# Kernel tuning notes

Hardware: AMD Instinct MI355X
Metric: run time of the kernel (lower is better)

The kernel has to match this reference:

```python
import jax, jax.numpy as jnp
import numpy as np

N_NODES = 100000
N_EDGES = 300000
N_GRAPHS = 2048
F_ATOM = 40
D_IN = 128    # GINInputSize
D_HID = 256   # GINHiddenSize
D_OUT = 512   # FPSize
D_TASK = 1    # OutputSize


def _glorot(key, shape):
    fan_in, fan_out = shape[0], shape[1]
    lim = (6.0 / (fan_in + fan_out)) ** 0.5
    return jax.random.uniform(key, shape, jnp.float32, -lim, lim)


def setup_inputs() -> dict:
    key = jax.random.key(0)
    ks = jax.random.split(key, 16)
    inp = {
        'x': jax.random.normal(ks[0], (N_NODES, F_ATOM), jnp.float32),
        'edge_index': jax.random.randint(ks[1], (2, N_EDGES), 0, N_NODES, jnp.int64),
        'batch': jnp.sort(jax.random.randint(ks[2], (N_NODES,), 0, N_GRAPHS, jnp.int64)),
        # NodeFeatEmbed: MLP([F_ATOM, D_IN]) == single Linear (plain_last)
        'W_embed': _glorot(ks[3], (F_ATOM, D_IN)),
        'b_embed': jnp.zeros((D_IN,), jnp.float32),
        # GINConv eps per layer (train_eps=False -> 0.0 constants)
        'eps': jnp.zeros((3,), jnp.float32),
        # layer 0: MLP([D_IN, D_HID, D_HID])
        'W1_0': _glorot(ks[4], (D_IN, D_HID)),  'b1_0': jnp.zeros((D_HID,), jnp.float32),
        'W2_0': _glorot(ks[5], (D_HID, D_HID)), 'b2_0': jnp.zeros((D_HID,), jnp.float32),
        # layer 1: MLP([D_HID, D_HID, D_HID])
        'W1_1': _glorot(ks[6], (D_HID, D_HID)), 'b1_1': jnp.zeros((D_HID,), jnp.float32),
        'W2_1': _glorot(ks[7], (D_HID, D_HID)), 'b2_1': jnp.zeros((D_HID,), jnp.float32),
        # layer 2 (last, maps to out_channels=FPSize): MLP([D_HID, D_OUT, D_OUT])
        'W1_2': _glorot(ks[8], (D_HID, D_OUT)), 'b1_2': jnp.zeros((D_OUT,), jnp.float32),
        'W2_2': _glorot(ks[9], (D_OUT, D_OUT)), 'b2_2': jnp.zeros((D_OUT,), jnp.float32),
        # task head
        'W_task': _glorot(ks[10], (D_OUT, D_TASK)),
        'b_task': jnp.zeros((D_TASK,), jnp.float32),
    }
    return inp


def _gin_forward(x, edge_index, batch, W_embed, b_embed, eps, layers, W_task, b_task):
    src, dst = edge_index[0], edge_index[1]
    # NodeFeatEmbed
    h = x @ W_embed + b_embed                                    # [N, D_IN]
    n_layers = len(layers)
    for l, (W1, b1, W2, b2) in enumerate(layers):
        # GINConv: MLP((1+eps)*h + sum_{j->i} h_j)
        agg = jax.ops.segment_sum(h[src], dst, num_segments=N_NODES)
        z = (1.0 + eps[l]) * h + agg
        h = jax.nn.relu(z @ W1 + b1) @ W2 + b2
        if l < n_layers - 1:                                     # inter-layer act (not after last)
            h = jax.nn.relu(h)
    # global_add_pool readout
    pooled = jax.ops.segment_sum(h, batch, num_segments=N_GRAPHS)  # [G, D_OUT]
    return pooled @ W_task + b_task                               # [G, D_TASK]


def reference(x, edge_index, batch, W_embed, b_embed, eps,
              W1_0, b1_0, W2_0, b2_0,
              W1_1, b1_1, W2_1, b2_1,
              W1_2, b1_2, W2_2, b2_2,
              W_task, b_task):
    layers = [(W1_0, b1_0, W2_0, b2_0), (W1_1, b1_1, W2_1, b2_1), (W1_2, b1_2, W2_2, b2_2)]
    return _gin_forward(x, edge_index, batch, W_embed, b_embed, eps, layers, W_task, b_task)
```

## Files before the change

kernel.cpp:

```cpp
#include <hip/hip_runtime.h>

#define N_NODES 100000
#define E_EDGES 300000
#define N_GRAPHS 2048

typedef float  floatx4 __attribute__((ext_vector_type(4)));
typedef short  shortx8 __attribute__((ext_vector_type(8)));

__device__ __forceinline__ float bf2f(unsigned short u) {
  return __uint_as_float(((unsigned int)u) << 16);
}
__device__ __forceinline__ unsigned short f2bf(float f) {
  unsigned int u = __float_as_uint(f);
  u += 0x7FFFu + ((u >> 16) & 1u);
  return (unsigned short)(u >> 16);
}

__device__ __forceinline__ void cp16(const void* g, void* l) {
  __builtin_amdgcn_global_load_lds(
      (const __attribute__((address_space(1))) unsigned int*)g,
      (__attribute__((address_space(3))) unsigned int*)l, 16, 0, 0);
}

struct PrepArgs {
  const float* W[4];
  unsigned short* Wt[4];
  int K[4];
  int N[4];
  const float* We;
  const float* be;
  const float* W1_0;
  unsigned short* WfT;
  const float* W2_2;
  const float* b2_2;
  const float* wtask;
  float* w2v;
  float* c2;
  float* nodedot;
  float* out;
  const float* b_task;
};

__global__ __launch_bounds__(256)
void prep_kernel(PrepArgs a) {
  const int blk = blockIdx.x;
  if (blk < 320) {
    int z, b;
    if (blk < 64)       { z = 0; b = blk; }
    else if (blk < 128) { z = 1; b = blk - 64; }
    else if (blk < 192) { z = 2; b = blk - 128; }
    else                { z = 3; b = blk - 192; }
    const int K = a.K[z], N = a.N[z];
    const int nt = N / 32;
    const int kb = (b / nt) * 32, nb = (b % nt) * 32;
    __shared__ unsigned short tile[32][33];
    const float* W = a.W[z];
    unsigned short* Wt = a.Wt[z];
    const int tx = threadIdx.x & 31, ty = threadIdx.x >> 5;
    for (int r = ty; r < 32; r += 8)
      tile[r][tx] = f2bf(W[(size_t)(kb + r) * N + nb + tx]);
    __syncthreads();
    for (int r = ty; r < 32; r += 8)
      Wt[(size_t)(nb + r) * K + kb + tx] = tile[tx][r];
  } else if (blk < 361) {
    const int k = blk - 320;
    const int n = threadIdx.x;
    if (k < 40) {
      float s = 0.f;
      for (int j = 0; j < 128; j++) s = fmaf(a.We[k * 128 + j], a.W1_0[(size_t)j * 256 + n], s);
      a.WfT[n * 64 + k] = f2bf(s);
    } else {
      float s = 0.f;
      for (int j = 0; j < 128; j++) s = fmaf(a.be[j], a.W1_0[(size_t)j * 256 + n], s);
      a.WfT[n * 64 + 40] = f2bf(s);
      for (int kk = 41; kk < 64; kk++) a.WfT[n * 64 + kk] = 0;
    }
  } else if (blk < 490) {
    const int p = blk - 361;
    const int lane = threadIdx.x & 63;
    const int wave = threadIdx.x >> 6;
    if (p < 128) {
      const int k = p * 4 + wave;
      const float* row = a.W2_2 + (size_t)k * 512 + lane * 8;
      float4 a0 = *(const float4*)(row);
      float4 a1 = *(const float4*)(row + 4);
      float4 w0 = *(const float4*)(a.wtask + lane * 8);
      float4 w1 = *(const float4*)(a.wtask + lane * 8 + 4);
      float s = a0.x * w0.x + a0.y * w0.y + a0.z * w0.z + a0.w * w0.w +
                a1.x * w1.x + a1.y * w1.y + a1.z * w1.z + a1.w * w1.w;
#pragma unroll
      for (int off = 32; off > 0; off >>= 1) s += __shfl_down(s, off);
      if (lane == 0) a.w2v[k] = s;
    } else if (wave == 0) {
      float4 a0 = *(const float4*)(a.b2_2 + lane * 8);
      float4 a1 = *(const float4*)(a.b2_2 + lane * 8 + 4);
      float4 w0 = *(const float4*)(a.wtask + lane * 8);
      float4 w1 = *(const float4*)(a.wtask + lane * 8 + 4);
      float s = a0.x * w0.x + a0.y * w0.y + a0.z * w0.z + a0.w * w0.w +
                a1.x * w1.x + a1.y * w1.y + a1.z * w1.z + a1.w * w1.w;
#pragma unroll
      for (int off = 32; off > 0; off >>= 1) s += __shfl_down(s, off);
      if (lane == 0) *a.c2 = s;
    }
  } else if (blk < 881) {
    int i = (blk - 490) * 256 + threadIdx.x;
    if (i < N_NODES) a.nodedot[i] = 0.f;
  } else {
    int g = (blk - 881) * 256 + threadIdx.x;
    if (g < N_GRAPHS) a.out[g] = a.b_task[0];
  }
}

__global__ __launch_bounds__(256)
void hist_kernel(const int* __restrict__ ei, int* __restrict__ deg) {
  int e = blockIdx.x * 256 + threadIdx.x;
  if (e < E_EDGES) atomicAdd(&deg[ei[E_EDGES + e]], 1);
}

__global__ __launch_bounds__(256)
void scan_blk_kernel(const int* __restrict__ in, int* __restrict__ out,
                     int* __restrict__ blk_sums, int n_in, int n_out) {
  __shared__ int sm[256];
  const int t = threadIdx.x;
  const int base = blockIdx.x * 1024 + t * 4;
  int d0 = (base + 0 < n_in) ? in[base + 0] : 0;
  int d1 = (base + 1 < n_in) ? in[base + 1] : 0;
  int d2 = (base + 2 < n_in) ? in[base + 2] : 0;
  int d3 = (base + 3 < n_in) ? in[base + 3] : 0;
  int s = d0 + d1 + d2 + d3;
  sm[t] = s;
  __syncthreads();
  for (int off = 1; off < 256; off <<= 1) {
    int v = (t >= off) ? sm[t - off] : 0;
    __syncthreads();
    sm[t] += v;
    __syncthreads();
  }
  int excl = sm[t] - s;
  if (base + 0 < n_out) out[base + 0] = excl;
  if (base + 1 < n_out) out[base + 1] = excl + d0;
  if (base + 2 < n_out) out[base + 2] = excl + d0 + d1;
  if (base + 3 < n_out) out[base + 3] = excl + d0 + d1 + d2;
  if (t == 255 && blk_sums) blk_sums[blockIdx.x] = sm[255];
}

__global__ __launch_bounds__(256)
void scan_fix_kernel(int* __restrict__ row_ptr, const int* __restrict__ blk_off,
                     int* __restrict__ cursor) {
  int i = blockIdx.x * 256 + threadIdx.x;
  if (i <= N_NODES) {
    int v = row_ptr[i] + blk_off[i >> 10];
    row_ptr[i] = v;
    if (i < N_NODES) cursor[i] = v;
  }
}

__global__ __launch_bounds__(256)
void fill_kernel(const int* __restrict__ ei, int* __restrict__ cursor,
                 int* __restrict__ csr_src) {
  int e = blockIdx.x * 256 + threadIdx.x;
  if (e < E_EDGES) {
    int d = ei[E_EDGES + e];
    int slot = atomicAdd(&cursor[d], 1);
    csr_src[slot] = ei[e];
  }
}

__global__ __launch_bounds__(256)
void gatherx_kernel(const float* __restrict__ X, unsigned short* __restrict__ G,
                    const int* __restrict__ row_ptr, const int* __restrict__ csr,
                    const float* __restrict__ eps) {
  const int node = blockIdx.x * 4 + (threadIdx.x >> 6);
  const int lane = threadIdx.x & 63;
  const float sc = 1.0f + eps[0];
  const int e0 = row_ptr[node];
  const int e1 = row_ptr[node + 1];
  float acc = 0.f;
  if (lane < 40) {
    acc = sc * X[(size_t)node * 40 + lane];
    int e = e0;
    for (; e + 4 <= e1; e += 4) {
      int s0 = csr[e], s1 = csr[e + 1], s2 = csr[e + 2], s3 = csr[e + 3];
      float a0 = X[(size_t)s0 * 40 + lane];
      float a1 = X[(size_t)s1 * 40 + lane];
      float a2 = X[(size_t)s2 * 40 + lane];
      float a3 = X[(size_t)s3 * 40 + lane];
      acc += (a0 + a1) + (a2 + a3);
    }
    for (; e < e1; e++)
      acc += X[(size_t)csr[e] * 40 + lane];
  } else if (lane == 40) {
    acc = sc + (float)(e1 - e0);
  }
  G[(size_t)node * 64 + lane] = f2bf(acc);
}

__global__ __launch_bounds__(256)
void gather_kernel(const unsigned short* __restrict__ H, unsigned short* __restrict__ Z,
                   const int* __restrict__ row_ptr, const int* __restrict__ csr,
                   const float* __restrict__ eps, int l) {
  const int node = blockIdx.x * 4 + (threadIdx.x >> 6);
  const int lane = threadIdx.x & 63;
  const int half = lane >> 5;
  const int hl = lane & 31;
  const float sc = 1.0f + eps[l];
  float acc[8];
#pragma unroll
  for (int k = 0; k < 8; k++) acc[k] = 0.f;

  if (half == 0) {
    uint4 v = *(const uint4*)(H + (size_t)node * 256 + hl * 8);
    acc[0] = sc * bf2f((unsigned short)(v.x & 0xFFFF));
    acc[1] = sc * bf2f((unsigned short)(v.x >> 16));
    acc[2] = sc * bf2f((unsigned short)(v.y & 0xFFFF));
    acc[3] = sc * bf2f((unsigned short)(v.y >> 16));
    acc[4] = sc * bf2f((unsigned short)(v.z & 0xFFFF));
    acc[5] = sc * bf2f((unsigned short)(v.z >> 16));
    acc[6] = sc * bf2f((unsigned short)(v.w & 0xFFFF));
    acc[7] = sc * bf2f((unsigned short)(v.w >> 16));
  }

  const int e0 = row_ptr[node];
  const int e1 = row_ptr[node + 1];
  int e = e0;
  for (; e + 2 <= e1; e += 2) {
    int s = csr[e + half];
    uint4 v = *(const uint4*)(H + (size_t)s * 256 + hl * 8);
    acc[0] += bf2f((unsigned short)(v.x & 0xFFFF));
    acc[1] += bf2f((unsigned short)(v.x >> 16));
    acc[2] += bf2f((unsigned short)(v.y & 0xFFFF));
    acc[3] += bf2f((unsigned short)(v.y >> 16));
    acc[4] += bf2f((unsigned short)(v.z & 0xFFFF));
    acc[5] += bf2f((unsigned short)(v.z >> 16));
    acc[6] += bf2f((unsigned short)(v.w & 0xFFFF));
    acc[7] += bf2f((unsigned short)(v.w >> 16));
  }
  if (e < e1 && half == 0) {
    int s = csr[e];
    uint4 v = *(const uint4*)(H + (size_t)s * 256 + hl * 8);
    acc[0] += bf2f((unsigned short)(v.x & 0xFFFF));
    acc[1] += bf2f((unsigned short)(v.x >> 16));
    acc[2] += bf2f((unsigned short)(v.y & 0xFFFF));
    acc[3] += bf2f((unsigned short)(v.y >> 16));
    acc[4] += bf2f((unsigned short)(v.z & 0xFFFF));
    acc[5] += bf2f((unsigned short)(v.z >> 16));
    acc[6] += bf2f((unsigned short)(v.w & 0xFFFF));
    acc[7] += bf2f((unsigned short)(v.w >> 16));
  }

#pragma unroll
  for (int k = 0; k < 8; k++) acc[k] += __shfl_down(acc[k], 32);

  if (half == 0) {
    unsigned short z[8];
#pragma unroll
    for (int k = 0; k < 8; k++) z[k] = f2bf(acc[k]);
    *(uint4*)(Z + (size_t)node * 256 + hl * 8) = *(const uint4*)z;
  }
}

template <int K1>
__global__ __launch_bounds__(256, 2)
void fused_mlp_kernel(const unsigned short* __restrict__ A,
                      const unsigned short* __restrict__ W1t,
                      const float* __restrict__ b1,
                      const unsigned short* __restrict__ W2t,
                      const float* __restrict__ b2,
                      unsigned short* __restrict__ H,
                      int M) {
  constexpr int ACH = K1 / 8;
  constexpr int ZP = (64 * ACH) / 256;
  constexpr int NT1 = K1 / 32;

  __shared__ unsigned short Bs[2][256 * 32];
  __shared__ unsigned short Ts[64 * 256];

  const int m0 = blockIdx.x * 64;
  const int tid = threadIdx.x;
  const int lane = tid & 63;
  const int wave = tid >> 6;
  const int fr = lane & 15;
  const int fq = lane >> 4;
  const int wn = wave * 64;

#pragma unroll
  for (int p = 0; p < ZP; p++) {
    int slot = p * 256 + tid;
    int row = slot / ACH;
    int cs = slot % ACH;
    int cg = cs ^ (row & 7);
    int grow = m0 + row;
    if (grow >= M) grow = M - 1;
    cp16(A + (size_t)grow * K1 + cg * 8, Ts + (size_t)(p * 256 + wn) * 8);
  }

  const int bn_ = tid >> 2;
  const int bc_ = tid & 3;
  const unsigned short* srcW1[4];
  const unsigned short* srcW2[4];
#pragma unroll
  for (int p = 0; p < 4; p++) {
    int n = p * 64 + bn_;
    int sw = (bc_ ^ ((n >> 1) & 3)) << 3;
    srcW1[p] = W1t + (size_t)n * K1 + sw;
    srcW2[p] = W2t + (size_t)n * 256 + sw;
  }

  int offB[4];
#pragma unroll
  for (int j = 0; j < 4; j++) {
    int n = wn + j * 16 + fr;
    offB[j] = n * 32 + ((fq ^ ((n >> 1) & 3)) << 3);
  }

#pragma unroll
  for (int p = 0; p < 4; p++)
    cp16(srcW1[p], &Bs[0][(size_t)(p * 256 + wn) * 8]);

  floatx4 acc[4][4];
#pragma unroll
  for (int i = 0; i < 4; i++)
#pragma unroll
    for (int j = 0; j < 4; j++) acc[i][j] = (floatx4){0.f, 0.f, 0.f, 0.f};

  __syncthreads();
  int buf = 0;

  for (int t = 0; t < NT1; t++) {
    if (t + 1 < NT1) {
#pragma unroll
      for (int p = 0; p < 4; p++)
        cp16(srcW1[p] + (t + 1) * 32, &Bs[buf ^ 1][(size_t)(p * 256 + wn) * 8]);
    } else {
#pragma unroll
      for (int p = 0; p < 4; p++)
        cp16(srcW2[p], &Bs[buf ^ 1][(size_t)(p * 256 + wn) * 8]);
    }
    shortx8 af[4], bv[4];
    const int kc = t * 4;
#pragma unroll
    for (int i = 0; i < 4; i++) {
      int row = i * 16 + fr;
      af[i] = *(const shortx8*)&Ts[row * K1 + (((kc + fq) ^ (fr & 7)) << 3)];
    }
#pragma unroll
    for (int j = 0; j < 4; j++) bv[j] = *(const shortx8*)&Bs[buf][offB[j]];
#pragma unroll
    for (int i = 0; i < 4; i++)
#pragma unroll
      for (int j = 0; j < 4; j++)
        acc[i][j] = __builtin_amdgcn_mfma_f32_16x16x32_bf16(af[i], bv[j], acc[i][j], 0, 0, 0);
    __syncthreads();
    buf ^= 1;
  }

#pragma unroll
  for (int j = 0; j < 4; j++) {
    int col = wn + j * 16 + fr;
    float bb = b1[col];
    int cgc = col >> 3, c7 = col & 7;
#pragma unroll
    for (int i = 0; i < 4; i++)
#pragma unroll
      for (int r = 0; r < 4; r++) {
        int row = i * 16 + fq * 4 + r;
        float v = fmaxf(acc[i][j][r] + bb, 0.f);
        Ts[row * 256 + (((cgc ^ (row & 7)) << 3) | c7)] = f2bf(v);
        acc[i][j][r] = 0.f;
      }
  }
  __syncthreads();

  for (int t = 0; t < 8; t++) {
    if (t + 1 < 8) {
#pragma unroll
      for (int p = 0; p < 4; p++)
        cp16(srcW2[p] + (t + 1) * 32, &Bs[buf ^ 1][(size_t)(p * 256 + wn) * 8]);
    }
    shortx8 af[4], bv[4];
    const int kc = t * 4;
#pragma unroll
    for (int i = 0; i < 4; i++) {
      int row = i * 16 + fr;
      af[i] = *(const shortx8*)&Ts[row * 256 + (((kc + fq) ^ (fr & 7)) << 3)];
    }
#pragma unroll
    for (int j = 0; j < 4; j++) bv[j] = *(const shortx8*)&Bs[buf][offB[j]];
#pragma unroll
    for (int i = 0; i < 4; i++)
#pragma unroll
      for (int j = 0; j < 4; j++)
        acc[i][j] = __builtin_amdgcn_mfma_f32_16x16x32_bf16(af[i], bv[j], acc[i][j], 0, 0, 0);
    __syncthreads();
    buf ^= 1;
  }

#pragma unroll
  for (int j = 0; j < 4; j++) {
    int col = wn + j * 16 + fr;
    float bb = b2[col];
    int cgc = col >> 3, c7 = col & 7;
#pragma unroll
    for (int i = 0; i < 4; i++)
#pragma unroll
      for (int r = 0; r < 4; r++) {
        int row = i * 16 + fq * 4 + r;
        float v = fmaxf(acc[i][j][r] + bb, 0.f);
        Ts[row * 256 + (((cgc ^ (row & 7)) << 3) | c7)] = f2bf(v);
      }
  }
  __syncthreads();
  const int r2 = tid >> 5;
  const int cg2 = tid & 31;
#pragma unroll
  for (int p = 0; p < 8; p++) {
    int row = p * 8 + r2;
    int grow = m0 + row;
    if (grow < M) {
      uint4 v = *(const uint4*)&Ts[row * 256 + ((cg2 ^ (row & 7)) << 3)];
      *(uint4*)&H[(size_t)grow * 256 + cg2 * 8] = v;
    }
  }
}

__global__ __launch_bounds__(256, 2)
void fused_dot_kernel(const unsigned short* __restrict__ A,
                      const unsigned short* __restrict__ W1t,
                      const float* __restrict__ b1,
                      const float* __restrict__ w2v,
                      float* __restrict__ nodedot4, int M) {
  __shared__ unsigned short Bs[2][256 * 32];
  __shared__ unsigned short Ts[64 * 256];

  const int m0 = blockIdx.x * 64;
  const int tid = threadIdx.x;
  const int lane = tid & 63;
  const int wave = tid >> 6;
  const int fr = lane & 15;
  const int fq = lane >> 4;
  const int wn = wave * 64;

#pragma unroll
  for (int p = 0; p < 8; p++) {
    int slot = p * 256 + tid;
    int row = slot >> 5;
    int cs = slot & 31;
    int cg = cs ^ (row & 7);
    int grow = m0 + row;
    if (grow >= M) grow = M - 1;
    cp16(A + (size_t)grow * 256 + cg * 8, Ts + (size_t)(p * 256 + wn) * 8);
  }

  const int bn_ = tid >> 2;
  const int bc_ = tid & 3;
  const unsigned short* srcW[4];
#pragma unroll
  for (int p = 0; p < 4; p++) {
    int n = p * 64 + bn_;
    srcW[p] = W1t + (size_t)n * 256 + ((bc_ ^ ((n >> 1) & 3)) << 3);
  }
  int offB[4];
#pragma unroll
  for (int j = 0; j < 4; j++) {
    int n = wn + j * 16 + fr;
    offB[j] = n * 32 + ((fq ^ ((n >> 1) & 3)) << 3);
  }

#pragma unroll
  for (int p = 0; p < 4; p++)
    cp16(srcW[p], &Bs[0][(size_t)(p * 256 + wn) * 8]);

  float pd[4][4];
#pragma unroll
  for (int i = 0; i < 4; i++)
#pragma unroll
    for (int r = 0; r < 4; r++) pd[i][r] = 0.f;

  floatx4 acc[4][4];
#pragma unroll
  for (int i = 0; i < 4; i++)
#pragma unroll
    for (int j = 0; j < 4; j++) acc[i][j] = (floatx4){0.f, 0.f, 0.f, 0.f};

  __syncthreads();
  int buf = 0;

  for (int s = 0; s < 16; s++) {
    int ns = s + 1;
    if (ns < 16) {
      const size_t off = (size_t)(ns >> 3) * 65536 + (size_t)(ns & 7) * 32;
#pragma unroll
      for (int p = 0; p < 4; p++)
        cp16(srcW[p] + off, &Bs[buf ^ 1][(size_t)(p * 256 + wn) * 8]);
    }
    shortx8 af[4], bv[4];
    const int kc = (s & 7) * 4;
#pragma unroll
    for (int i = 0; i < 4; i++) {
      int row = i * 16 + fr;
      af[i] = *(const shortx8*)&Ts[row * 256 + (((kc + fq) ^ (fr & 7)) << 3)];
    }
#pragma unroll
    for (int j = 0; j < 4; j++) bv[j] = *(const shortx8*)&Bs[buf][offB[j]];
#pragma unroll
    for (int i = 0; i < 4; i++)
#pragma unroll
      for (int j = 0; j < 4; j++)
        acc[i][j] = __builtin_amdgcn_mfma_f32_16x16x32_bf16(af[i], bv[j], acc[i][j], 0, 0, 0);
    __syncthreads();
    buf ^= 1;

    if ((s & 7) == 7) {
      const int nh = s >> 3;
#pragma unroll
      for (int j = 0; j < 4; j++) {
        int col = nh * 256 + wn + j * 16 + fr;
        float bb = b1[col];
        float wv = w2v[col];
#pragma unroll
        for (int i = 0; i < 4; i++)
#pragma unroll
          for (int r = 0; r < 4; r++) {
            pd[i][r] += fmaxf(acc[i][j][r] + bb, 0.f) * wv;
            acc[i][j][r] = 0.f;
          }
      }
    }
  }

#pragma unroll
  for (int i = 0; i < 4; i++)
#pragma unroll
    for (int r = 0; r < 4; r++) {
      float s = pd[i][r];
#pragma unroll
      for (int off = 1; off < 16; off <<= 1) s += __shfl_xor(s, off);
      if (fr == 0) {
        int row = m0 + i * 16 + fq * 4 + r;
        if (row < M) nodedot4[(size_t)wave * N_NODES + row] = s;
      }
    }
}

__global__ __launch_bounds__(256)
void pool_kernel(const float* __restrict__ nodedot4, const int* __restrict__ batch,
                 float* __restrict__ out, const float* __restrict__ c2p) {
  const int i = blockIdx.x * 256 + threadIdx.x;
  if (i >= N_NODES) return;
  const int lane = threadIdx.x & 63;
  const float c2 = *c2p;
  float v = (nodedot4[i] + nodedot4[N_NODES + i]) +
            (nodedot4[2 * N_NODES + i] + nodedot4[3 * N_NODES + i]) + c2;
  const int g = batch[i];
  float s = v;
#pragma unroll
  for (int off = 1; off < 64; off <<= 1) {
    float u = __shfl_up(s, off);
    int gu = __shfl_up(g, off);
    if (lane >= off && gu == g) s += u;
  }
  bool last = (i == N_NODES - 1) || (batch[i + 1] != g) || (lane == 63);
  if (last) unsafeAtomicAdd(&out[g], s);
}

extern "C" void kernel_launch(void* const* d_in, const int* in_sizes, int n_in,
                              void* d_out, int out_size, void* d_ws, size_t ws_size,
                              hipStream_t stream) {
  const float* x       = (const float*)d_in[0];
  const int*   ei      = (const int*)d_in[1];
  const int*   batch   = (const int*)d_in[2];
  const float* W_embed = (const float*)d_in[3];
  const float* b_embed = (const float*)d_in[4];
  const float* eps     = (const float*)d_in[5];
  const float* W1[3] = {(const float*)d_in[6],  (const float*)d_in[10], (const float*)d_in[14]};
  const float* B1[3] = {(const float*)d_in[7],  (const float*)d_in[11], (const float*)d_in[15]};
  const float* W2[3] = {(const float*)d_in[8],  (const float*)d_in[12], (const float*)d_in[16]};
  const float* B2[3] = {(const float*)d_in[9],  (const float*)d_in[13], (const float*)d_in[17]};
  const float* W_task = (const float*)d_in[18];
  const float* b_task = (const float*)d_in[19];
  float* out = (float*)d_out;

  const size_t OFF_ND4 = 51200000;
  const size_t OFF_RZ  = 102400000;
  const size_t OFF_AUX = 153600000;
  if (ws_size < OFF_AUX + 4000000) return;
  unsigned short* RH = (unsigned short*)d_ws;
  float* nodedot4 = (float*)((char*)d_ws + OFF_ND4);
  unsigned short* RZ = (unsigned short*)((char*)d_ws + OFF_RZ);
  char* aux = (char*)d_ws + OFF_AUX;
  int* row_ptr  = (int*)(aux);
  int* cursor   = (int*)(aux + 400016);
  int* csr_src  = (int*)(aux + 800016);
  int* blk_sums = (int*)(aux + 2000016);
  int* blk_off  = (int*)(aux + 2000416);
  unsigned short* WT = (unsigned short*)(aux + 2400832);
  float* w2v = (float*)(aux + 3200832);
  float* c2  = (float*)(aux + 3202880);
  unsigned short* WfT    = WT;
  unsigned short* Wt2_0  = WT + 32768;
  unsigned short* Wt1_1  = WT + 98304;
  unsigned short* Wt2_1  = WT + 163840;
  unsigned short* Wt1_2  = WT + 229376;

  PrepArgs pa;
  pa.W[0] = W2[0]; pa.Wt[0] = Wt2_0; pa.K[0] = 256; pa.N[0] = 256;
  pa.W[1] = W1[1]; pa.Wt[1] = Wt1_1; pa.K[1] = 256; pa.N[1] = 256;
  pa.W[2] = W2[1]; pa.Wt[2] = Wt2_1; pa.K[2] = 256; pa.N[2] = 256;
  pa.W[3] = W1[2]; pa.Wt[3] = Wt1_2; pa.K[3] = 256; pa.N[3] = 512;
  pa.We = W_embed; pa.be = b_embed; pa.W1_0 = W1[0]; pa.WfT = WfT;
  pa.W2_2 = W2[2]; pa.b2_2 = B2[2]; pa.wtask = W_task; pa.w2v = w2v; pa.c2 = c2;
  pa.nodedot = (float*)cursor;
  pa.out = out; pa.b_task = b_task;
  prep_kernel<<<889, 256, 0, stream>>>(pa);

  hist_kernel<<<(E_EDGES + 255) / 256, 256, 0, stream>>>(ei, cursor);
  scan_blk_kernel<<<98, 256, 0, stream>>>(cursor, row_ptr, blk_sums, N_NODES, N_NODES + 1);
  scan_blk_kernel<<<1, 256, 0, stream>>>(blk_sums, blk_off, nullptr, 98, 98);
  scan_fix_kernel<<<(N_NODES + 256) / 256, 256, 0, stream>>>(row_ptr, blk_off, cursor);
  fill_kernel<<<(E_EDGES + 255) / 256, 256, 0, stream>>>(ei, cursor, csr_src);

  const int FB = (N_NODES + 63) / 64;

  gatherx_kernel<<<N_NODES / 4, 256, 0, stream>>>(x, RZ, row_ptr, csr_src, eps);
  fused_mlp_kernel<64><<<FB, 256, 0, stream>>>(RZ, WfT, B1[0], Wt2_0, B2[0], RH, N_NODES);

  gather_kernel<<<N_NODES / 4, 256, 0, stream>>>(RH, RZ, row_ptr, csr_src, eps, 1);
  fused_mlp_kernel<256><<<FB, 256, 0, stream>>>(RZ, Wt1_1, B1[1], Wt2_1, B2[1], RH, N_NODES);

  gather_kernel<<<N_NODES / 4, 256, 0, stream>>>(RH, RZ, row_ptr, csr_src, eps, 2);
  fused_dot_kernel<<<FB, 256, 0, stream>>>(RZ, Wt1_2, B1[2], w2v, nodedot4, N_NODES);

  pool_kernel<<<(N_NODES + 255) / 256, 256, 0, stream>>>(nodedot4, batch, out, c2);
}
```

Measured before the change: 397.5 us.

## Single-buffer weight tiles via register staging to fit three blocks per CU

Both fused MLP kernels drop the double-buffered LDS weight tile and instead prefetch the next weight chunk into registers, writing it into a single LDS buffer between two barriers each step. The two GEMM loops of the MLP kernel are merged into one fully unrolled stage loop, and launch bounds rise from 2 to 3 blocks per CU to use the freed LDS. This aims to raise occupancy and hide latency, at the cost of an extra barrier per step, more register pressure, and synchronous global-to-register loads replacing async LDS copies.

```diff
diff --git a/kernel.cpp b/kernel.cpp
--- a/kernel.cpp
+++ b/kernel.cpp
@@ -260,7 +260,7 @@
 }
 
 template <int K1>
-__global__ __launch_bounds__(256, 2)
+__global__ __launch_bounds__(256, 3)
 void fused_mlp_kernel(const unsigned short* __restrict__ A,
                       const unsigned short* __restrict__ W1t,
                       const float* __restrict__ b1,
@@ -271,8 +271,9 @@
   constexpr int ACH = K1 / 8;
   constexpr int ZP = (64 * ACH) / 256;
   constexpr int NT1 = K1 / 32;
-
-  __shared__ unsigned short Bs[2][256 * 32];
+  constexpr int S = NT1 + 8;
+
+  __shared__ unsigned short Bs[256 * 32];
   __shared__ unsigned short Ts[64 * 256];
 
   const int m0 = blockIdx.x * 64;
@@ -305,6 +306,7 @@
     srcW1[p] = W1t + (size_t)n * K1 + sw;
     srcW2[p] = W2t + (size_t)n * 256 + sw;
   }
+#define PSRC(s, p) ((s) < NT1 ? srcW1[p] + (s) * 32 : srcW2[p] + ((s) - NT1) * 32)
 
   int offB[4];
 #pragma unroll
@@ -315,7 +317,10 @@
 
 #pragma unroll
   for (int p = 0; p < 4; p++)
-    cp16(srcW1[p], &Bs[0][(size_t)(p * 256 + wn) * 8]);
+    cp16(PSRC(0, p), &Bs[(size_t)(p * 256 + wn) * 8]);
+  uint4 rg[4];
+#pragma unroll
+  for (int p = 0; p < 4; p++) rg[p] = *(const uint4*)PSRC(1, p);
 
   floatx4 acc[4][4];
 #pragma unroll
@@ -324,76 +329,58 @@
     for (int j = 0; j < 4; j++) acc[i][j] = (floatx4){0.f, 0.f, 0.f, 0.f};
 
   __syncthreads();
-  int buf = 0;
-
-  for (int t = 0; t < NT1; t++) {
-    if (t + 1 < NT1) {
-#pragma unroll
-      for (int p = 0; p < 4; p++)
-        cp16(srcW1[p] + (t + 1) * 32, &Bs[buf ^ 1][(size_t)(p * 256 + wn) * 8]);
-    } else {
-#pragma unroll
-      for (int p = 0; p < 4; p++)
-        cp16(srcW2[p], &Bs[buf ^ 1][(size_t)(p * 256 + wn) * 8]);
-    }
+
+#pragma unroll
+  for (int s = 0; s < S; s++) {
     shortx8 af[4], bv[4];
-    const int kc = t * 4;
+    const int str = (s < NT1) ? K1 : 256;
+    const int kc = ((s < NT1) ? s : s - NT1) * 4;
 #pragma unroll
     for (int i = 0; i < 4; i++) {
       int row = i * 16 + fr;
-      af[i] = *(const shortx8*)&Ts[row * K1 + (((kc + fq) ^ (fr & 7)) << 3)];
-    }
-#pragma unroll
-    for (int j = 0; j < 4; j++) bv[j] = *(const shortx8*)&Bs[buf][offB[j]];
+      af[i] = *(const shortx8*)&Ts[row * str + (((kc + fq) ^ (fr & 7)) << 3)];
+    }
+#pragma unroll
+    for (int j = 0; j < 4; j++) bv[j] = *(const shortx8*)&Bs[offB[j]];
 #pragma unroll
     for (int i = 0; i < 4; i++)
 #pragma unroll
       for (int j = 0; j < 4; j++)
         acc[i][j] = __builtin_amdgcn_mfma_f32_16x16x32_bf16(af[i], bv[j], acc[i][j], 0, 0, 0);
+
     __syncthreads();
-    buf ^= 1;
-  }
-
-#pragma unroll
-  for (int j = 0; j < 4; j++) {
-    int col = wn + j * 16 + fr;
-    float bb = b1[col];
-    int cgc = col >> 3, c7 = col & 7;
-#pragma unroll
-    for (int i = 0; i < 4; i++)
-#pragma unroll
-      for (int r = 0; r < 4; r++) {
-        int row = i * 16 + fq * 4 + r;
-        float v = fmaxf(acc[i][j][r] + bb, 0.f);
-        Ts[row * 256 + (((cgc ^ (row & 7)) << 3) | c7)] = f2bf(v);
-        acc[i][j][r] = 0.f;
+
+    if (s == NT1 - 1) {
+#pragma unroll
+      for (int j = 0; j < 4; j++) {
+        int col = wn + j * 16 + fr;
+        float bb = b1[col];
+        int cgc = col >> 3, c7 = col & 7;
+#pragma unroll
+        for (int i = 0; i < 4; i++)
+#pragma unroll
+          for (int r = 0; r < 4; r++) {
+            int row = i * 16 + fq * 4 + r;
+            float v = fmaxf(acc[i][j][r] + bb, 0.f);
+            Ts[row * 256 + (((cgc ^ (row & 7)) << 3) | c7)] = f2bf(v);
+            acc[i][j][r] = 0.f;
+          }
       }
-  }
-  __syncthreads();
-
-  for (int t = 0; t < 8; t++) {
-    if (t + 1 < 8) {
+    }
+
+    if (s + 1 < S) {
 #pragma unroll
       for (int p = 0; p < 4; p++)
-        cp16(srcW2[p] + (t + 1) * 32, &Bs[buf ^ 1][(size_t)(p * 256 + wn) * 8]);
-    }
-    shortx8 af[4], bv[4];
-    const int kc = t * 4;
-#pragma unroll
-    for (int i = 0; i < 4; i++) {
-      int row = i * 16 + fr;
-      af[i] = *(const shortx8*)&Ts[row * 256 + (((kc + fq) ^ (fr & 7)) << 3)];
-    }
-#pragma unroll
-    for (int j = 0; j < 4; j++) bv[j] = *(const shortx8*)&Bs[buf][offB[j]];
-#pragma unroll
-    for (int i = 0; i < 4; i++)
-#pragma unroll
-      for (int j = 0; j < 4; j++)
-        acc[i][j] = __builtin_amdgcn_mfma_f32_16x16x32_bf16(af[i], bv[j], acc[i][j], 0, 0, 0);
+        *(uint4*)&Bs[(size_t)(p * 256 + tid) * 8] = rg[p];
+    }
     __syncthreads();
-    buf ^= 1;
-  }
+
+    if (s + 2 < S) {
+#pragma unroll
+      for (int p = 0; p < 4; p++) rg[p] = *(const uint4*)PSRC(s + 2, p);
+    }
+  }
+#undef PSRC
 
 #pragma unroll
   for (int j = 0; j < 4; j++) {
@@ -423,13 +410,13 @@
   }
 }
 
-__global__ __launch_bounds__(256, 2)
+__global__ __launch_bounds__(256, 3)
 void fused_dot_kernel(const unsigned short* __restrict__ A,
                       const unsigned short* __restrict__ W1t,
                       const float* __restrict__ b1,
                       const float* __restrict__ w2v,
                       float* __restrict__ nodedot4, int M) {
-  __shared__ unsigned short Bs[2][256 * 32];
+  __shared__ unsigned short Bs[256 * 32];
   __shared__ unsigned short Ts[64 * 256];
 
   const int m0 = blockIdx.x * 64;
@@ -459,6 +446,7 @@
     int n = p * 64 + bn_;
     srcW[p] = W1t + (size_t)n * 256 + ((bc_ ^ ((n >> 1) & 3)) << 3);
   }
+#define DSRC(s, p) (srcW[p] + (size_t)((s) >> 3) * 65536 + (size_t)((s) & 7) * 32)
   int offB[4];
 #pragma unroll
   for (int j = 0; j < 4; j++) {
@@ -468,7 +456,10 @@
 
 #pragma unroll
   for (int p = 0; p < 4; p++)
-    cp16(srcW[p], &Bs[0][(size_t)(p * 256 + wn) * 8]);
+    cp16(DSRC(0, p), &Bs[(size_t)(p * 256 + wn) * 8]);
+  uint4 rg[4];
+#pragma unroll
+  for (int p = 0; p < 4; p++) rg[p] = *(const uint4*)DSRC(1, p);
 
   float pd[4][4];
 #pragma unroll
@@ -483,16 +474,9 @@
     for (int j = 0; j < 4; j++) acc[i][j] = (floatx4){0.f, 0.f, 0.f, 0.f};
 
   __syncthreads();
-  int buf = 0;
-
+
+#pragma unroll
   for (int s = 0; s < 16; s++) {
-    int ns = s + 1;
-    if (ns < 16) {
-      const size_t off = (size_t)(ns >> 3) * 65536 + (size_t)(ns & 7) * 32;
-#pragma unroll
-      for (int p = 0; p < 4; p++)
-        cp16(srcW[p] + off, &Bs[buf ^ 1][(size_t)(p * 256 + wn) * 8]);
-    }
     shortx8 af[4], bv[4];
     const int kc = (s & 7) * 4;
 #pragma unroll
@@ -501,14 +485,12 @@
       af[i] = *(const shortx8*)&Ts[row * 256 + (((kc + fq) ^ (fr & 7)) << 3)];
     }
 #pragma unroll
-    for (int j = 0; j < 4; j++) bv[j] = *(const shortx8*)&Bs[buf][offB[j]];
+    for (int j = 0; j < 4; j++) bv[j] = *(const shortx8*)&Bs[offB[j]];
 #pragma unroll
     for (int i = 0; i < 4; i++)
 #pragma unroll
       for (int j = 0; j < 4; j++)
         acc[i][j] = __builtin_amdgcn_mfma_f32_16x16x32_bf16(af[i], bv[j], acc[i][j], 0, 0, 0);
-    __syncthreads();
-    buf ^= 1;
 
     if ((s & 7) == 7) {
       const int nh = s >> 3;
@@ -526,7 +508,20 @@
           }
       }
     }
-  }
+
+    __syncthreads();
+    if (s + 1 < 16) {
+#pragma unroll
+      for (int p = 0; p < 4; p++)
+        *(uint4*)&Bs[(size_t)(p * 256 + tid) * 8] = rg[p];
+    }
+    __syncthreads();
+    if (s + 2 < 16) {
+#pragma unroll
+      for (int p = 0; p < 4; p++) rg[p] = *(const uint4*)DSRC(s + 2, p);
+    }
+  }
+#undef DSRC
 
 #pragma unroll
   for (int i = 0; i < 4; i++)
```

After: 615.9 us. 54.9% more time.
